# Performance work log

Measured on AMD Instinct MI355X. Metric: run time of the kernel, lower is better.

The kernel has to match this reference:

```python
import jax, jax.numpy as jnp
import numpy as np

B, T, C, H = 8, 1024, 768, 12
D = C // H  # head_dim = 64

def _rope_tables(seq_len, d, base=10000.0):
    inv_freq = 1.0 / (base ** (jnp.arange(0, d, 2, dtype=jnp.float32) / d))  # [d/2]
    freqs = jnp.outer(jnp.arange(seq_len, dtype=jnp.float32), inv_freq)      # [T, d/2]
    return jnp.cos(freqs), jnp.sin(freqs)

def _apply_rotary(x, cos, sin):
    # x: [B,T,H,D]; cos/sin: [1,T,1,D/2]
    d = x.shape[-1] // 2
    x1, x2 = x[..., :d], x[..., d:]
    return jnp.concatenate([x1 * cos + x2 * sin, -x1 * sin + x2 * cos], axis=-1)

def setup_inputs() -> dict:
    key = jax.random.key(0)
    k1, k2, k3 = jax.random.split(key, 3)
    x = jax.random.normal(k1, (B, T, C), dtype=jnp.float32)
    w_qkv = jax.random.normal(k2, (3 * C, C), dtype=jnp.float32) * (C ** -0.5)
    w_proj = jax.random.normal(k3, (C, C), dtype=jnp.float32) * (C ** -0.5)
    return {"x": x, "w_qkv": w_qkv, "w_proj": w_proj}

def reference(x, w_qkv, w_proj):
    Bb, Tt, Cc = x.shape
    qkv = x @ w_qkv.T                                   # [B,T,3C]
    q, k, v = jnp.split(qkv, 3, axis=2)
    q = q.reshape(Bb, Tt, H, D)
    k = k.reshape(Bb, Tt, H, D)
    v = v.reshape(Bb, Tt, H, D)
    cos, sin = _rope_tables(Tt, D)
    cos = cos[None, :, None, :]
    sin = sin[None, :, None, :]
    q = _apply_rotary(q, cos, sin)
    k = _apply_rotary(k, cos, sin)
    scale = 1.0 / jnp.sqrt(jnp.float32(D))
    scores = jnp.einsum('bthd,bshd->bhts', q, k) * scale  # [B,H,T,T]
    causal = jnp.tril(jnp.ones((Tt, Tt), dtype=bool))
    scores = jnp.where(causal[None, None], scores, jnp.finfo(scores.dtype).min)
    p = jax.nn.softmax(scores, axis=-1)
    y = jnp.einsum('bhts,bshd->bthd', p, v).reshape(Bb, Tt, Cc)
    return y @ w_proj.T
```

## Files before the change

### kernel.cpp

```cpp
#include <hip/hip_runtime.h>
#include <hip/hip_bf16.h>

#define Bb 8
#define Tt 1024
#define Cc 768
#define Hh 12
#define Dd 64
#define M_ROWS (Bb * Tt)
#define QKV_N (3 * Cc)

typedef __attribute__((ext_vector_type(8))) short s16x8;
typedef __attribute__((ext_vector_type(4))) short s16x4;
typedef __attribute__((ext_vector_type(4))) float f32x4;

#define AS1 __attribute__((address_space(1)))
#define AS3 __attribute__((address_space(3)))

static __device__ __forceinline__ short f2bf(float f) {
    union { float f; unsigned u; } v; v.f = f;
    unsigned r = (v.u + 0x7fffu + ((v.u >> 16) & 1u)) >> 16;
    return (short)r;
}
static __device__ __forceinline__ unsigned pkt(float hi, float lo) {
    union { float f; unsigned u; } a, b; a.f = hi; b.f = lo;
    return __builtin_amdgcn_perm(a.u, b.u, 0x07060302u);
}

static __device__ __forceinline__ void cast8(const float* __restrict__ in,
                                             short* __restrict__ out, int i) {
    const float4 a = ((const float4*)in)[i * 2];
    const float4 b = ((const float4*)in)[i * 2 + 1];
    s16x8 f;
    f[0] = f2bf(a.x); f[1] = f2bf(a.y); f[2] = f2bf(a.z); f[3] = f2bf(a.w);
    f[4] = f2bf(b.x); f[5] = f2bf(b.y); f[6] = f2bf(b.z); f[7] = f2bf(b.w);
    ((s16x8*)out)[i] = f;
}

#define S1 (M_ROWS * Cc / 8)
#define S2 (QKV_N * Cc / 8)
#define S3 (Cc * Cc / 8)
#define SROPE (Tt * 32)
#define PREP_THREADS (S1 + S2 + S3 + SROPE)

__global__ __launch_bounds__(256) void prep_kernel(const float* __restrict__ x,
                                                   const float* __restrict__ wqkv,
                                                   const float* __restrict__ wproj,
                                                   short* __restrict__ xb,
                                                   short* __restrict__ wqkvb,
                                                   short* __restrict__ wprojb,
                                                   float2* __restrict__ cs) {
    int idx = blockIdx.x * blockDim.x + threadIdx.x;
    if (idx < S1) { cast8(x, xb, idx); return; }
    idx -= S1;
    if (idx < S2) {
        int row = idx / 96;
        int c8  = idx - row * 96;
        int q2 = (row >> 4) & 3;
        int src = (row < 2 * Cc && (q2 == 1 || q2 == 2)) ? (row ^ 0x30) : row;
        const float4 a = ((const float4*)(wqkv + (size_t)src * Cc))[c8 * 2];
        const float4 b = ((const float4*)(wqkv + (size_t)src * Cc))[c8 * 2 + 1];
        s16x8 f;
        f[0] = f2bf(a.x); f[1] = f2bf(a.y); f[2] = f2bf(a.z); f[3] = f2bf(a.w);
        f[4] = f2bf(b.x); f[5] = f2bf(b.y); f[6] = f2bf(b.z); f[7] = f2bf(b.w);
        ((s16x8*)wqkvb)[idx] = f;
        return;
    }
    idx -= S2;
    if (idx < S3) { cast8(wproj, wprojb, idx); return; }
    idx -= S3;
    {
        int t = idx >> 5, i = idx & 31;
        float inv_freq = exp2f(-0.41524101186092037f * (float)i);
        float fr = (float)t * inv_freq;
        float2 v; v.x = cosf(fr); v.y = sinf(fr);
        cs[idx] = v;
    }
}

template <int MODE, int TN>
__global__ __launch_bounds__(256, 3) void gemm_nt_mfma(const short* __restrict__ A,
                                                       const short* __restrict__ B,
                                                       void* __restrict__ Cout,
                                                       const float2* __restrict__ cs,
                                                       int M, int N, int K, int nblocks) {
    __shared__ short As[2][128 * 32];
    __shared__ short Bs[2][TN * 32];
    constexpr int NTW = TN / 32;

    const int wave = threadIdx.x >> 6;
    const int lane = threadIdx.x & 63;
    const int l16  = lane & 15;
    const int quad = lane >> 4;
    const int wr = wave >> 1;
    const int wc = wave & 1;

    const int mb8  = (M >> 7) >> 3;
    const int xcd  = blockIdx.x & 7;
    const int slot = blockIdx.x >> 3;
    const int bm = (xcd * mb8 + slot / nblocks) * 128;
    const int bn = (slot % nblocks) * TN;

    f32x4 acc[4][NTW] = {};

    auto stage = [&](int k0, int buf) {
#pragma unroll
        for (int j = 0; j < 2; j++) {
            const int D = j * 256 + wave * 64 + lane;
            const int G = D >> 3;
            const int s = (G << 3) | ((D & 7) ^ (G & 7));
            const int m = s >> 2, c4 = (s & 3) * 8;
            __builtin_amdgcn_global_load_lds(
                (const AS1 unsigned*)(A + (size_t)(bm + m) * K + k0 + c4),
                (AS3 unsigned*)&As[buf][(j * 256 + wave * 64) * 8], 16, 0, 0);
        }
        constexpr int BCH = TN * 4;
#pragma unroll
        for (int j = 0; j < (BCH + 255) / 256; j++) {
            if (BCH % 256 == 0 || j * 256 + wave * 64 < BCH) {
                const int D = j * 256 + wave * 64 + lane;
                const int G = D >> 3;
                const int s = (G << 3) | ((D & 7) ^ (G & 7));
                const int m = s >> 2, c4 = (s & 3) * 8;
                __builtin_amdgcn_global_load_lds(
                    (const AS1 unsigned*)(B + (size_t)(bn + m) * K + k0 + c4),
                    (AS3 unsigned*)&Bs[buf][(j * 256 + wave * 64) * 8], 16, 0, 0);
            }
        }
    };

    const int nIter = K >> 5;
    stage(0, 0);
    for (int kt = 0; kt < nIter; kt++) {
        const int buf = kt & 1;
        __syncthreads();
        if (kt + 1 < nIter) stage((kt + 1) << 5, buf ^ 1);

        s16x8 af[4];
#pragma unroll
        for (int mt = 0; mt < 4; mt++) {
            const int m = wr * 64 + mt * 16 + l16;
            const int d = ((m & 1) * 4 + quad) ^ ((m >> 1) & 7);
            af[mt] = *(const s16x8*)&As[buf][(m >> 1) * 64 + d * 8];
        }
#pragma unroll
        for (int nt = 0; nt < NTW; nt++) {
            const int n = wc * (TN / 2) + nt * 16 + l16;
            const int d = ((n & 1) * 4 + quad) ^ ((n >> 1) & 7);
            s16x8 bf = *(const s16x8*)&Bs[buf][(n >> 1) * 64 + d * 8];
#pragma unroll
            for (int mt = 0; mt < 4; mt++)
                acc[mt][nt] = __builtin_amdgcn_mfma_f32_16x16x32_bf16(
                    af[mt], bf, acc[mt][nt], 0, 0, 0);
        }
    }

    if constexpr (MODE == 0) {
#pragma unroll
        for (int mt = 0; mt < 4; mt++)
#pragma unroll
            for (int r = 0; r < 4; r++) {
                const size_t row = bm + wr * 64 + mt * 16 + quad * 4 + r;
#pragma unroll
                for (int nt = 0; nt < NTW; nt++)
                    ((float*)Cout)[row * N + bn + wc * (TN / 2) + nt * 16 + l16] =
                        acc[mt][nt][r];
            }
    } else {
        const bool is_v = (bn >= 2 * Cc);
        if (is_v) {
#pragma unroll
            for (int mt = 0; mt < 4; mt++)
#pragma unroll
                for (int r = 0; r < 4; r++) {
                    const size_t row = bm + wr * 64 + mt * 16 + quad * 4 + r;
#pragma unroll
                    for (int nt = 0; nt < NTW; nt++)
                        ((short*)Cout)[row * N + bn + wc * (TN / 2) + nt * 16 + l16] =
                            f2bf(acc[mt][nt][r]);
                }
        } else {
            const float scale = (bn < Cc) ? 0.125f : 1.0f;
#pragma unroll
            for (int mt = 0; mt < 4; mt++) {
#pragma unroll
                for (int r = 0; r < 4; r++) {
                    const int row = bm + wr * 64 + mt * 16 + quad * 4 + r;
                    const int t = row & (Tt - 1);
                    short* cp = (short*)Cout + (size_t)row * N + bn + wc * (TN / 2);
#pragma unroll
                    for (int p = 0; p < NTW; p += 2) {
                        const int g = wc * NTW + p;
                        const int i0 = ((g & 2) ? 16 : 0) + l16;
                        const float2 c0 = cs[t * 32 + i0];
                        const float x1 = acc[mt][p][r];
                        const float x2 = acc[mt][p + 1][r];
                        cp[p * 16 + l16]        = f2bf((x1 * c0.x + x2 * c0.y) * scale);
                        cp[(p + 1) * 16 + l16]  = f2bf((-x1 * c0.y + x2 * c0.x) * scale);
                    }
                }
            }
        }
    }
}

template <int TN>
__global__ __launch_bounds__(256, 2) void gemm_nt_proj2(const short* __restrict__ A,
                                                        const short* __restrict__ B,
                                                        float* __restrict__ Cout,
                                                        int M, int N, int K, int nblocks) {
    __shared__ short As[2][2][128 * 32];
    __shared__ short Bs[2][2][TN * 32];
    constexpr int NTW = TN / 32;

    const int wave = threadIdx.x >> 6;
    const int lane = threadIdx.x & 63;
    const int l16  = lane & 15;
    const int quad = lane >> 4;
    const int wr = wave >> 1;
    const int wc = wave & 1;

    const int mb8  = (M >> 7) >> 3;
    const int xcd  = blockIdx.x & 7;
    const int slot = blockIdx.x >> 3;
    const int bm = (xcd * mb8 + slot / nblocks) * 128;
    const int bn = (slot % nblocks) * TN;

    f32x4 acc[4][NTW] = {};

    auto stage = [&](int k0, int p, int t) {
#pragma unroll
        for (int j = 0; j < 2; j++) {
            const int D = j * 256 + wave * 64 + lane;
            const int G = D >> 3;
            const int s = (G << 3) | ((D & 7) ^ (G & 7));
            const int m = s >> 2, c4 = (s & 3) * 8;
            __builtin_amdgcn_global_load_lds(
                (const AS1 unsigned*)(A + (size_t)(bm + m) * K + k0 + c4),
                (AS3 unsigned*)&As[p][t][(j * 256 + wave * 64) * 8], 16, 0, 0);
        }
        constexpr int BCH = TN * 4;
#pragma unroll
        for (int j = 0; j < (BCH + 255) / 256; j++) {
            if (BCH % 256 == 0 || j * 256 + wave * 64 < BCH) {
                const int D = j * 256 + wave * 64 + lane;
                const int G = D >> 3;
                const int s = (G << 3) | ((D & 7) ^ (G & 7));
                const int m = s >> 2, c4 = (s & 3) * 8;
                __builtin_amdgcn_global_load_lds(
                    (const AS1 unsigned*)(B + (size_t)(bn + m) * K + k0 + c4),
                    (AS3 unsigned*)&Bs[p][t][(j * 256 + wave * 64) * 8], 16, 0, 0);
            }
        }
    };

    const int nPair = K >> 6;
    stage(0, 0, 0);
    stage(32, 0, 1);
    for (int it = 0; it < nPair; it++) {
        const int p = it & 1;
        __syncthreads();
        if (it + 1 < nPair) {
            stage((2 * it + 2) << 5, p ^ 1, 0);
            stage((2 * it + 3) << 5, p ^ 1, 1);
        }
#pragma unroll
        for (int t = 0; t < 2; t++) {
            s16x8 af[4];
#pragma unroll
            for (int mt = 0; mt < 4; mt++) {
                const int m = wr * 64 + mt * 16 + l16;
                const int d = ((m & 1) * 4 + quad) ^ ((m >> 1) & 7);
                af[mt] = *(const s16x8*)&As[p][t][(m >> 1) * 64 + d * 8];
            }
#pragma unroll
            for (int nt = 0; nt < NTW; nt++) {
                const int n = wc * (TN / 2) + nt * 16 + l16;
                const int d = ((n & 1) * 4 + quad) ^ ((n >> 1) & 7);
                s16x8 bf = *(const s16x8*)&Bs[p][t][(n >> 1) * 64 + d * 8];
#pragma unroll
                for (int mt = 0; mt < 4; mt++)
                    acc[mt][nt] = __builtin_amdgcn_mfma_f32_16x16x32_bf16(
                        af[mt], bf, acc[mt][nt], 0, 0, 0);
            }
        }
    }

#pragma unroll
    for (int mt = 0; mt < 4; mt++)
#pragma unroll
        for (int r = 0; r < 4; r++) {
            const size_t row = bm + wr * 64 + mt * 16 + quad * 4 + r;
#pragma unroll
            for (int nt = 0; nt < NTW; nt++)
                Cout[row * N + bn + wc * (TN / 2) + nt * 16 + l16] = acc[mt][nt][r];
        }
}

#define KSP 72
#define VSP 72

__global__ __launch_bounds__(256, 3) void flash_attn(const short* __restrict__ qkv,
                                                     short* __restrict__ y) {
    __shared__ short Ks[2][64 * KSP];
    __shared__ short Vs[2][64 * VSP];

    const int wave = threadIdx.x >> 6;
    const int lane = threadIdx.x & 63;
    const int l16  = lane & 15;
    const int quad = lane >> 4;

    const int pair = blockIdx.x / 96;
    const int bh   = blockIdx.x % 96;
    const int h = bh % Hh;
    const int b = bh / Hh;
    const int qa_blk = pair;
    const int qb_blk = 15 - pair;
    const int q0a = qa_blk * 64 + wave * 16;
    const int q0b = qb_blk * 64 + wave * 16;

    s16x8 qfa[2], qfb[2];
    {
        const short* qpa = qkv + (size_t)(b * Tt + q0a + l16) * QKV_N + h * Dd + quad * 8;
        const short* qpb = qkv + (size_t)(b * Tt + q0b + l16) * QKV_N + h * Dd + quad * 8;
        qfa[0] = *(const s16x8*)qpa;  qfa[1] = *(const s16x8*)(qpa + 32);
        qfb[0] = *(const s16x8*)qpb;  qfb[1] = *(const s16x8*)(qpb + 32);
    }

    f32x4 oa[4] = {}, ob[4] = {};
    float la = 0.f, lb = 0.f;

    const int krow = threadIdx.x >> 2;
    const int kd0  = (threadIdx.x & 3) * 16;
    const int key2 = (threadIdx.x & 31) * 2;
    const int dv0  = (threadIdx.x >> 5) * 8;

    s16x8 pk0, pk1, pv0, pv1;
    auto load_tile = [&](int kbase) {
        const short* kp = qkv + (size_t)(b * Tt + kbase + krow) * QKV_N + Cc + h * Dd + kd0;
        pk0 = *(const s16x8*)kp;
        pk1 = *(const s16x8*)(kp + 8);
        const short* vp = qkv + (size_t)(b * Tt + kbase + key2) * QKV_N + 2 * Cc + h * Dd + dv0;
        pv0 = *(const s16x8*)vp;
        pv1 = *(const s16x8*)(vp + QKV_N);
    };
    auto store_tile = [&](int buf) {
        *(s16x8*)&Ks[buf][krow * KSP + kd0]     = pk0;
        *(s16x8*)&Ks[buf][krow * KSP + kd0 + 8] = pk1;
#pragma unroll
        for (int j = 0; j < 8; j++) {
            ushort2 w; w.x = (unsigned short)pv0[j]; w.y = (unsigned short)pv1[j];
            *(ushort2*)&Vs[buf][(dv0 + j) * VSP + key2] = w;
        }
    };

    auto process_pair = [&](int buf, int kbase, bool mask_a) {
        short* pwb = &Ks[buf ^ 1][wave * 16 * KSP];
        short* pwa = &Vs[buf ^ 1][wave * 16 * VSP];
        f32x4 eb[4], ea[4];
        __builtin_amdgcn_s_setprio(1);
#pragma unroll
        for (int g = 0; g < 4; g++) {
            s16x8 kf0 = *(const s16x8*)&Ks[buf][(g * 16 + l16) * KSP + quad * 8];
            s16x8 kf1 = *(const s16x8*)&Ks[buf][(g * 16 + l16) * KSP + 32 + quad * 8];
            f32x4 zb = {}, za = {};
            zb = __builtin_amdgcn_mfma_f32_16x16x32_bf16(kf0, qfb[0], zb, 0, 0, 0);
            zb = __builtin_amdgcn_mfma_f32_16x16x32_bf16(kf1, qfb[1], zb, 0, 0, 0);
            za = __builtin_amdgcn_mfma_f32_16x16x32_bf16(kf0, qfa[0], za, 0, 0, 0);
            za = __builtin_amdgcn_mfma_f32_16x16x32_bf16(kf1, qfa[1], za, 0, 0, 0);
            eb[g] = zb; ea[g] = za;
        }
        __builtin_amdgcn_s_setprio(0);
        float rsb = 0.f, rsa = 0.f;
#pragma unroll
        for (int g = 0; g < 4; g++) {
#pragma unroll
            for (int r = 0; r < 4; r++) {
                float pb = __expf(eb[g][r]); rsb += pb; eb[g][r] = pb;
                float pa = __expf(ea[g][r]);
                if (mask_a) pa = (kbase + g * 16 + quad * 4 + r <= q0a + l16) ? pa : 0.0f;
                rsa += pa; ea[g][r] = pa;
            }
            uint2 ub, ua;
            ub.x = pkt(eb[g][1], eb[g][0]); ub.y = pkt(eb[g][3], eb[g][2]);
            ua.x = pkt(ea[g][1], ea[g][0]); ua.y = pkt(ea[g][3], ea[g][2]);
            *(uint2*)&pwb[l16 * KSP + g * 16 + quad * 4] = ub;
            *(uint2*)&pwa[l16 * VSP + g * 16 + quad * 4] = ua;
        }
        lb += rsb; la += rsa;
        __builtin_amdgcn_s_setprio(1);
#pragma unroll
        for (int c = 0; c < 2; c++) {
            s16x8 pbb = *(const s16x8*)&pwb[l16 * KSP + c * 32 + quad * 8];
            s16x8 pba = *(const s16x8*)&pwa[l16 * VSP + c * 32 + quad * 8];
#pragma unroll
            for (int nc = 0; nc < 4; nc++) {
                s16x8 vb = *(const s16x8*)&Vs[buf][(nc * 16 + l16) * VSP + c * 32 + quad * 8];
                ob[nc] = __builtin_amdgcn_mfma_f32_16x16x32_bf16(vb, pbb, ob[nc], 0, 0, 0);
                oa[nc] = __builtin_amdgcn_mfma_f32_16x16x32_bf16(vb, pba, oa[nc], 0, 0, 0);
            }
        }
        __builtin_amdgcn_s_setprio(0);
    };

    auto process_single = [&](int buf, int kbase, bool masked) {
        short* pw = &Ks[buf ^ 1][wave * 16 * KSP];
        f32x4 e[4];
        __builtin_amdgcn_s_setprio(1);
#pragma unroll
        for (int g = 0; g < 4; g++) {
            s16x8 kf0 = *(const s16x8*)&Ks[buf][(g * 16 + l16) * KSP + quad * 8];
            s16x8 kf1 = *(const s16x8*)&Ks[buf][(g * 16 + l16) * KSP + 32 + quad * 8];
            f32x4 z = {};
            z = __builtin_amdgcn_mfma_f32_16x16x32_bf16(kf0, qfb[0], z, 0, 0, 0);
            z = __builtin_amdgcn_mfma_f32_16x16x32_bf16(kf1, qfb[1], z, 0, 0, 0);
            e[g] = z;
        }
        __builtin_amdgcn_s_setprio(0);
        float rs = 0.f;
#pragma unroll
        for (int g = 0; g < 4; g++) {
#pragma unroll
            for (int r = 0; r < 4; r++) {
                float p = __expf(e[g][r]);
                if (masked) p = (kbase + g * 16 + quad * 4 + r <= q0b + l16) ? p : 0.0f;
                rs += p; e[g][r] = p;
            }
            uint2 u;
            u.x = pkt(e[g][1], e[g][0]); u.y = pkt(e[g][3], e[g][2]);
            *(uint2*)&pw[l16 * KSP + g * 16 + quad * 4] = u;
        }
        lb += rs;
        __builtin_amdgcn_s_setprio(1);
#pragma unroll
        for (int c = 0; c < 2; c++) {
            s16x8 pb = *(const s16x8*)&pw[l16 * KSP + c * 32 + quad * 8];
#pragma unroll
            for (int nc = 0; nc < 4; nc++) {
                s16x8 vb = *(const s16x8*)&Vs[buf][(nc * 16 + l16) * VSP + c * 32 + quad * 8];
                ob[nc] = __builtin_amdgcn_mfma_f32_16x16x32_bf16(vb, pb, ob[nc], 0, 0, 0);
            }
        }
        __builtin_amdgcn_s_setprio(0);
    };

    load_tile(0);
    store_tile(0);
    for (int kt = 0; kt <= qb_blk; kt++) {
        __syncthreads();
        const int nb = (kt < qb_blk) ? (kt + 1) * 64 : qb_blk * 64;
        load_tile(nb);
        const int buf = kt & 1;
        const int kbase = kt * 64;
        if (kt <= qa_blk)
            process_pair(buf, kbase, kt == qa_blk);
        else
            process_single(buf, kbase, kt == qb_blk);
        store_tile(buf ^ 1);
    }

    float sa = la; sa += __shfl_xor(sa, 16, 64); sa += __shfl_xor(sa, 32, 64);
    float sb = lb; sb += __shfl_xor(sb, 16, 64); sb += __shfl_xor(sb, 32, 64);
    const float inva = 1.0f / sa;
    const float invb = 1.0f / sb;
    short* ypa = y + (size_t)(b * Tt + q0a + l16) * Cc + h * Dd + quad * 4;
    short* ypb = y + (size_t)(b * Tt + q0b + l16) * Cc + h * Dd + quad * 4;
#pragma unroll
    for (int nc = 0; nc < 4; nc++) {
        s16x4 va, vb2;
#pragma unroll
        for (int r = 0; r < 4; r++) {
            va[r]  = f2bf(oa[nc][r] * inva);
            vb2[r] = f2bf(ob[nc][r] * invb);
        }
        *(s16x4*)&ypa[nc * 16] = va;
        *(s16x4*)&ypb[nc * 16] = vb2;
    }
}

extern "C" void kernel_launch(void* const* d_in, const int* in_sizes, int n_in,
                              void* d_out, int out_size, void* d_ws, size_t ws_size,
                              hipStream_t stream) {
    const float* x      = (const float*)d_in[0];
    const float* w_qkv  = (const float*)d_in[1];
    const float* w_proj = (const float*)d_in[2];
    float* out = (float*)d_out;

    float2* cs    = (float2*)d_ws;
    short* xb     = (short*)(cs + Tt * 32);
    short* wqkvb  = xb + (size_t)M_ROWS * Cc;
    short* wprojb = wqkvb + (size_t)QKV_N * Cc;
    short* qkvb   = wprojb + (size_t)Cc * Cc;
    short* yb     = qkvb + (size_t)M_ROWS * QKV_N;

    prep_kernel<<<PREP_THREADS / 256, 256, 0, stream>>>(
        x, w_qkv, w_proj, xb, wqkvb, wprojb, cs);

    gemm_nt_mfma<1, 192><<<768, 256, 0, stream>>>(
        xb, wqkvb, qkvb, cs, M_ROWS, QKV_N, Cc, QKV_N / 192);

    flash_attn<<<96 * 8, 256, 0, stream>>>(qkvb, yb);

    gemm_nt_proj2<96><<<512, 256, 0, stream>>>(
        yb, wprojb, out, M_ROWS, Cc, Cc, Cc / 96);
}
```

Measured before the change: 163.2 us.

## Give each attention wave 32 query rows and use exp2 with folded log2e scale

After: 187.6 us. 1.15x slower.

```diff
diff --git a/kernel.cpp b/kernel.cpp
--- a/kernel.cpp
+++ b/kernel.cpp
@@ -179,7 +179,7 @@
                             f2bf(acc[mt][nt][r]);
                 }
         } else {
-            const float scale = (bn < Cc) ? 0.125f : 1.0f;
+            const float scale = (bn < Cc) ? 0.18033688511112043f : 1.0f;
 #pragma unroll
             for (int mt = 0; mt < 4; mt++) {
 #pragma unroll
@@ -299,7 +299,7 @@
 #define KSP 72
 #define VSP 72
 
-__global__ __launch_bounds__(256, 3) void flash_attn(const short* __restrict__ qkv,
+__global__ __launch_bounds__(128, 2) void flash_attn(const short* __restrict__ qkv,
                                                      short* __restrict__ y) {
     __shared__ short Ks[2][64 * KSP];
     __shared__ short Vs[2][64 * VSP];
@@ -315,129 +315,164 @@
     const int b = bh / Hh;
     const int qa_blk = pair;
     const int qb_blk = 15 - pair;
-    const int q0a = qa_blk * 64 + wave * 16;
-    const int q0b = qb_blk * 64 + wave * 16;
-
-    s16x8 qfa[2], qfb[2];
-    {
-        const short* qpa = qkv + (size_t)(b * Tt + q0a + l16) * QKV_N + h * Dd + quad * 8;
-        const short* qpb = qkv + (size_t)(b * Tt + q0b + l16) * QKV_N + h * Dd + quad * 8;
-        qfa[0] = *(const s16x8*)qpa;  qfa[1] = *(const s16x8*)(qpa + 32);
-        qfb[0] = *(const s16x8*)qpb;  qfb[1] = *(const s16x8*)(qpb + 32);
-    }
-
-    f32x4 oa[4] = {}, ob[4] = {};
-    float la = 0.f, lb = 0.f;
-
-    const int krow = threadIdx.x >> 2;
-    const int kd0  = (threadIdx.x & 3) * 16;
+    const int q0a = qa_blk * 64 + wave * 32;
+    const int q0b = qb_blk * 64 + wave * 32;
+
+    s16x8 qfa[2][2], qfb[2][2];
+#pragma unroll
+    for (int f = 0; f < 2; f++) {
+        const short* qpa = qkv + (size_t)(b * Tt + q0a + f * 16 + l16) * QKV_N + h * Dd + quad * 8;
+        const short* qpb = qkv + (size_t)(b * Tt + q0b + f * 16 + l16) * QKV_N + h * Dd + quad * 8;
+        qfa[f][0] = *(const s16x8*)qpa;  qfa[f][1] = *(const s16x8*)(qpa + 32);
+        qfb[f][0] = *(const s16x8*)qpb;  qfb[f][1] = *(const s16x8*)(qpb + 32);
+    }
+
+    f32x4 oa[2][4] = {}, ob[2][4] = {};
+    float la[2] = {0.f, 0.f}, lb[2] = {0.f, 0.f};
+
+    const int krow = threadIdx.x >> 1;
+    const int kd0  = (threadIdx.x & 1) * 32;
     const int key2 = (threadIdx.x & 31) * 2;
-    const int dv0  = (threadIdx.x >> 5) * 8;
-
-    s16x8 pk0, pk1, pv0, pv1;
+    const int dv0  = (threadIdx.x >> 5) * 16;
+
+    s16x8 pk0, pk1, pk2, pk3, pv00, pv01, pv10, pv11;
     auto load_tile = [&](int kbase) {
         const short* kp = qkv + (size_t)(b * Tt + kbase + krow) * QKV_N + Cc + h * Dd + kd0;
         pk0 = *(const s16x8*)kp;
         pk1 = *(const s16x8*)(kp + 8);
+        pk2 = *(const s16x8*)(kp + 16);
+        pk3 = *(const s16x8*)(kp + 24);
         const short* vp = qkv + (size_t)(b * Tt + kbase + key2) * QKV_N + 2 * Cc + h * Dd + dv0;
-        pv0 = *(const s16x8*)vp;
-        pv1 = *(const s16x8*)(vp + QKV_N);
+        pv00 = *(const s16x8*)vp;
+        pv01 = *(const s16x8*)(vp + 8);
+        pv10 = *(const s16x8*)(vp + QKV_N);
+        pv11 = *(const s16x8*)(vp + QKV_N + 8);
     };
     auto store_tile = [&](int buf) {
-        *(s16x8*)&Ks[buf][krow * KSP + kd0]     = pk0;
-        *(s16x8*)&Ks[buf][krow * KSP + kd0 + 8] = pk1;
+        *(s16x8*)&Ks[buf][krow * KSP + kd0]      = pk0;
+        *(s16x8*)&Ks[buf][krow * KSP + kd0 + 8]  = pk1;
+        *(s16x8*)&Ks[buf][krow * KSP + kd0 + 16] = pk2;
+        *(s16x8*)&Ks[buf][krow * KSP + kd0 + 24] = pk3;
 #pragma unroll
         for (int j = 0; j < 8; j++) {
-            ushort2 w; w.x = (unsigned short)pv0[j]; w.y = (unsigned short)pv1[j];
+            ushort2 w; w.x = (unsigned short)pv00[j]; w.y = (unsigned short)pv10[j];
             *(ushort2*)&Vs[buf][(dv0 + j) * VSP + key2] = w;
         }
+#pragma unroll
+        for (int j = 0; j < 8; j++) {
+            ushort2 w; w.x = (unsigned short)pv01[j]; w.y = (unsigned short)pv11[j];
+            *(ushort2*)&Vs[buf][(dv0 + 8 + j) * VSP + key2] = w;
+        }
     };
 
     auto process_pair = [&](int buf, int kbase, bool mask_a) {
-        short* pwb = &Ks[buf ^ 1][wave * 16 * KSP];
-        short* pwa = &Vs[buf ^ 1][wave * 16 * VSP];
-        f32x4 eb[4], ea[4];
+        short* pwb = &Ks[buf ^ 1][wave * 32 * KSP];
+        short* pwa = &Vs[buf ^ 1][wave * 32 * VSP];
+        f32x4 eb[2][4], ea[2][4];
         __builtin_amdgcn_s_setprio(1);
 #pragma unroll
         for (int g = 0; g < 4; g++) {
             s16x8 kf0 = *(const s16x8*)&Ks[buf][(g * 16 + l16) * KSP + quad * 8];
             s16x8 kf1 = *(const s16x8*)&Ks[buf][(g * 16 + l16) * KSP + 32 + quad * 8];
-            f32x4 zb = {}, za = {};
-            zb = __builtin_amdgcn_mfma_f32_16x16x32_bf16(kf0, qfb[0], zb, 0, 0, 0);
-            zb = __builtin_amdgcn_mfma_f32_16x16x32_bf16(kf1, qfb[1], zb, 0, 0, 0);
-            za = __builtin_amdgcn_mfma_f32_16x16x32_bf16(kf0, qfa[0], za, 0, 0, 0);
-            za = __builtin_amdgcn_mfma_f32_16x16x32_bf16(kf1, qfa[1], za, 0, 0, 0);
-            eb[g] = zb; ea[g] = za;
+#pragma unroll
+            for (int f = 0; f < 2; f++) {
+                f32x4 zb = {}, za = {};
+                zb = __builtin_amdgcn_mfma_f32_16x16x32_bf16(kf0, qfb[f][0], zb, 0, 0, 0);
+                zb = __builtin_amdgcn_mfma_f32_16x16x32_bf16(kf1, qfb[f][1], zb, 0, 0, 0);
+                za = __builtin_amdgcn_mfma_f32_16x16x32_bf16(kf0, qfa[f][0], za, 0, 0, 0);
+                za = __builtin_amdgcn_mfma_f32_16x16x32_bf16(kf1, qfa[f][1], za, 0, 0, 0);
+                eb[f][g] = zb; ea[f][g] = za;
+            }
         }
         __builtin_amdgcn_s_setprio(0);
-        float rsb = 0.f, rsa = 0.f;
-#pragma unroll
-        for (int g = 0; g < 4; g++) {
-#pragma unroll
-            for (int r = 0; r < 4; r++) {
-                float pb = __expf(eb[g][r]); rsb += pb; eb[g][r] = pb;
-                float pa = __expf(ea[g][r]);
-                if (mask_a) pa = (kbase + g * 16 + quad * 4 + r <= q0a + l16) ? pa : 0.0f;
-                rsa += pa; ea[g][r] = pa;
-            }
-            uint2 ub, ua;
-            ub.x = pkt(eb[g][1], eb[g][0]); ub.y = pkt(eb[g][3], eb[g][2]);
-            ua.x = pkt(ea[g][1], ea[g][0]); ua.y = pkt(ea[g][3], ea[g][2]);
-            *(uint2*)&pwb[l16 * KSP + g * 16 + quad * 4] = ub;
-            *(uint2*)&pwa[l16 * VSP + g * 16 + quad * 4] = ua;
-        }
-        lb += rsb; la += rsa;
+#pragma unroll
+        for (int f = 0; f < 2; f++) {
+            float rsb = 0.f, rsa = 0.f;
+#pragma unroll
+            for (int g = 0; g < 4; g++) {
+#pragma unroll
+                for (int r = 0; r < 4; r++) {
+                    float pb = exp2f(eb[f][g][r]); rsb += pb; eb[f][g][r] = pb;
+                    float pa = exp2f(ea[f][g][r]);
+                    if (mask_a) pa = (kbase + g * 16 + quad * 4 + r <= q0a + f * 16 + l16) ? pa : 0.0f;
+                    rsa += pa; ea[f][g][r] = pa;
+                }
+                uint2 ub, ua;
+                ub.x = pkt(eb[f][g][1], eb[f][g][0]); ub.y = pkt(eb[f][g][3], eb[f][g][2]);
+                ua.x = pkt(ea[f][g][1], ea[f][g][0]); ua.y = pkt(ea[f][g][3], ea[f][g][2]);
+                *(uint2*)&pwb[(f * 16 + l16) * KSP + g * 16 + quad * 4] = ub;
+                *(uint2*)&pwa[(f * 16 + l16) * VSP + g * 16 + quad * 4] = ua;
+            }
+            lb[f] += rsb; la[f] += rsa;
+        }
         __builtin_amdgcn_s_setprio(1);
 #pragma unroll
         for (int c = 0; c < 2; c++) {
-            s16x8 pbb = *(const s16x8*)&pwb[l16 * KSP + c * 32 + quad * 8];
-            s16x8 pba = *(const s16x8*)&pwa[l16 * VSP + c * 32 + quad * 8];
-#pragma unroll
-            for (int nc = 0; nc < 4; nc++) {
-                s16x8 vb = *(const s16x8*)&Vs[buf][(nc * 16 + l16) * VSP + c * 32 + quad * 8];
-                ob[nc] = __builtin_amdgcn_mfma_f32_16x16x32_bf16(vb, pbb, ob[nc], 0, 0, 0);
-                oa[nc] = __builtin_amdgcn_mfma_f32_16x16x32_bf16(vb, pba, oa[nc], 0, 0, 0);
+            s16x8 vbf[4];
+#pragma unroll
+            for (int nc = 0; nc < 4; nc++)
+                vbf[nc] = *(const s16x8*)&Vs[buf][(nc * 16 + l16) * VSP + c * 32 + quad * 8];
+#pragma unroll
+            for (int f = 0; f < 2; f++) {
+                s16x8 pbb = *(const s16x8*)&pwb[(f * 16 + l16) * KSP + c * 32 + quad * 8];
+                s16x8 pba = *(const s16x8*)&pwa[(f * 16 + l16) * VSP + c * 32 + quad * 8];
+#pragma unroll
+                for (int nc = 0; nc < 4; nc++) {
+                    ob[f][nc] = __builtin_amdgcn_mfma_f32_16x16x32_bf16(vbf[nc], pbb, ob[f][nc], 0, 0, 0);
+                    oa[f][nc] = __builtin_amdgcn_mfma_f32_16x16x32_bf16(vbf[nc], pba, oa[f][nc], 0, 0, 0);
+                }
             }
         }
         __builtin_amdgcn_s_setprio(0);
     };
 
     auto process_single = [&](int buf, int kbase, bool masked) {
-        short* pw = &Ks[buf ^ 1][wave * 16 * KSP];
-        f32x4 e[4];
+        short* pw = &Ks[buf ^ 1][wave * 32 * KSP];
+        f32x4 e[2][4];
         __builtin_amdgcn_s_setprio(1);
 #pragma unroll
         for (int g = 0; g < 4; g++) {
             s16x8 kf0 = *(const s16x8*)&Ks[buf][(g * 16 + l16) * KSP + quad * 8];
             s16x8 kf1 = *(const s16x8*)&Ks[buf][(g * 16 + l16) * KSP + 32 + quad * 8];
-            f32x4 z = {};
-            z = __builtin_amdgcn_mfma_f32_16x16x32_bf16(kf0, qfb[0], z, 0, 0, 0);
-            z = __builtin_amdgcn_mfma_f32_16x16x32_bf16(kf1, qfb[1], z, 0, 0, 0);
-            e[g] = z;
+#pragma unroll
+            for (int f = 0; f < 2; f++) {
+                f32x4 z = {};
+                z = __builtin_amdgcn_mfma_f32_16x16x32_bf16(kf0, qfb[f][0], z, 0, 0, 0);
+                z = __builtin_amdgcn_mfma_f32_16x16x32_bf16(kf1, qfb[f][1], z, 0, 0, 0);
+                e[f][g] = z;
+            }
         }
         __builtin_amdgcn_s_setprio(0);
-        float rs = 0.f;
-#pragma unroll
-        for (int g = 0; g < 4; g++) {
-#pragma unroll
-            for (int r = 0; r < 4; r++) {
-                float p = __expf(e[g][r]);
-                if (masked) p = (kbase + g * 16 + quad * 4 + r <= q0b + l16) ? p : 0.0f;
-                rs += p; e[g][r] = p;
-            }
-            uint2 u;
-            u.x = pkt(e[g][1], e[g][0]); u.y = pkt(e[g][3], e[g][2]);
-            *(uint2*)&pw[l16 * KSP + g * 16 + quad * 4] = u;
-        }
-        lb += rs;
+#pragma unroll
+        for (int f = 0; f < 2; f++) {
+            float rs = 0.f;
+#pragma unroll
+            for (int g = 0; g < 4; g++) {
+#pragma unroll
+                for (int r = 0; r < 4; r++) {
+                    float p = exp2f(e[f][g][r]);
+                    if (masked) p = (kbase + g * 16 + quad * 4 + r <= q0b + f * 16 + l16) ? p : 0.0f;
+                    rs += p; e[f][g][r] = p;
+                }
+                uint2 u;
+                u.x = pkt(e[f][g][1], e[f][g][0]); u.y = pkt(e[f][g][3], e[f][g][2]);
+                *(uint2*)&pw[(f * 16 + l16) * KSP + g * 16 + quad * 4] = u;
+            }
+            lb[f] += rs;
+        }
         __builtin_amdgcn_s_setprio(1);
 #pragma unroll
         for (int c = 0; c < 2; c++) {
-            s16x8 pb = *(const s16x8*)&pw[l16 * KSP + c * 32 + quad * 8];
-#pragma unroll
-            for (int nc = 0; nc < 4; nc++) {
-                s16x8 vb = *(const s16x8*)&Vs[buf][(nc * 16 + l16) * VSP + c * 32 + quad * 8];
-                ob[nc] = __builtin_amdgcn_mfma_f32_16x16x32_bf16(vb, pb, ob[nc], 0, 0, 0);
+            s16x8 vbf[4];
+#pragma unroll
+            for (int nc = 0; nc < 4; nc++)
+                vbf[nc] = *(const s16x8*)&Vs[buf][(nc * 16 + l16) * VSP + c * 32 + quad * 8];
+#pragma unroll
+            for (int f = 0; f < 2; f++) {
+                s16x8 pb = *(const s16x8*)&pw[(f * 16 + l16) * KSP + c * 32 + quad * 8];
+#pragma unroll
+                for (int nc = 0; nc < 4; nc++)
+                    ob[f][nc] = __builtin_amdgcn_mfma_f32_16x16x32_bf16(vbf[nc], pb, ob[f][nc], 0, 0, 0);
             }
         }
         __builtin_amdgcn_s_setprio(0);
@@ -458,22 +493,25 @@
         store_tile(buf ^ 1);
     }
 
-    float sa = la; sa += __shfl_xor(sa, 16, 64); sa += __shfl_xor(sa, 32, 64);
-    float sb = lb; sb += __shfl_xor(sb, 16, 64); sb += __shfl_xor(sb, 32, 64);
-    const float inva = 1.0f / sa;
-    const float invb = 1.0f / sb;
-    short* ypa = y + (size_t)(b * Tt + q0a + l16) * Cc + h * Dd + quad * 4;
-    short* ypb = y + (size_t)(b * Tt + q0b + l16) * Cc + h * Dd + quad * 4;
-#pragma unroll
-    for (int nc = 0; nc < 4; nc++) {
-        s16x4 va, vb2;
-#pragma unroll
-        for (int r = 0; r < 4; r++) {
-            va[r]  = f2bf(oa[nc][r] * inva);
-            vb2[r] = f2bf(ob[nc][r] * invb);
-        }
-        *(s16x4*)&ypa[nc * 16] = va;
-        *(s16x4*)&ypb[nc * 16] = vb2;
+#pragma unroll
+    for (int f = 0; f < 2; f++) {
+        float sa = la[f]; sa += __shfl_xor(sa, 16, 64); sa += __shfl_xor(sa, 32, 64);
+        float sb = lb[f]; sb += __shfl_xor(sb, 16, 64); sb += __shfl_xor(sb, 32, 64);
+        const float inva = 1.0f / sa;
+        const float invb = 1.0f / sb;
+        short* ypa = y + (size_t)(b * Tt + q0a + f * 16 + l16) * Cc + h * Dd + quad * 4;
+        short* ypb = y + (size_t)(b * Tt + q0b + f * 16 + l16) * Cc + h * Dd + quad * 4;
+#pragma unroll
+        for (int nc = 0; nc < 4; nc++) {
+            s16x4 va, vb2;
+#pragma unroll
+            for (int r = 0; r < 4; r++) {
+                va[r]  = f2bf(oa[f][nc][r] * inva);
+                vb2[r] = f2bf(ob[f][nc][r] * invb);
+            }
+            *(s16x4*)&ypa[nc * 16] = va;
+            *(s16x4*)&ypb[nc * 16] = vb2;
+        }
     }
 }
 
@@ -498,7 +536,7 @@
     gemm_nt_mfma<1, 192><<<768, 256, 0, stream>>>(
         xb, wqkvb, qkvb, cs, M_ROWS, QKV_N, Cc, QKV_N / 192);
 
-    flash_attn<<<96 * 8, 256, 0, stream>>>(qkvb, yb);
+    flash_attn<<<96 * 8, 128, 0, stream>>>(qkvb, yb);
 
     gemm_nt_proj2<96><<<512, 256, 0, stream>>>(
         yb, wprojb, out, M_ROWS, Cc, Cc, Cc / 96);
```
